# Optimization experiments

Hardware: AMD Instinct MI355X
Metric: run time of the kernel (lower is better)

The kernel has to match this reference:

```python
import jax, jax.numpy as jnp
import numpy as np

B, S, D, R, N_IN, N_PROC, K = 4, 4096, 1024, 128, 8, 32, 4

def setup_inputs() -> dict:
    key = jax.random.key(0)
    k1, k2, k3, k4, k5 = jax.random.split(key, 5)
    x = jax.random.normal(k1, (B, S, D), dtype=jnp.float32)
    input_weights = jax.random.uniform(k2, (B, S, N_IN), dtype=jnp.float32)
    process_indices = jax.random.randint(k3, (B, S, K), 0, N_PROC, dtype=jnp.int32)
    # params: orthogonal-ish init approximated by scaled gaussian
    input_neurons = jax.random.normal(k4, (N_IN, D, R), dtype=jnp.float32) / np.sqrt(D).astype(np.float32)
    process_neurons = jax.random.normal(k5, (N_PROC, R), dtype=jnp.float32)
    process_neurons = process_neurons / (jnp.linalg.norm(process_neurons, axis=-1, keepdims=True) + 1e-8)
    return {"x": x, "input_weights": input_weights, "process_indices": process_indices,
            "input_neurons": input_neurons, "process_neurons": process_neurons}

def reference(x, input_weights, process_indices, input_neurons, process_neurons):
    # soft routing over input neurons: project with all N_IN matrices, weight, sum
    all_proj = jnp.einsum('bsd,ndr->bsnr', x, input_neurons)      # [B,S,N_IN,R]
    y = jnp.einsum('bsnr,bsn->bsr', all_proj, input_weights)       # [B,S,R]
    # gather per-token Householder vectors: [B,S,K,R]
    selected_v = process_neurons[process_indices]
    # sequential chain of K Householder reflections via scan over the K axis
    def step(xc, v):
        # v: [B,S,R]
        v_norm_sq = jnp.sum(v * v, axis=-1, keepdims=True) + 1e-8
        vn = v / jnp.sqrt(v_norm_sq)
        vTx = jnp.sum(xc * vn, axis=-1, keepdims=True)
        return xc - 2.0 * vn * vTx, None
    out, _ = jax.lax.scan(step, y, jnp.moveaxis(selected_v, 2, 0))
    return out
```

## Files before the change

kernel.cpp:

```cpp
#include <hip/hip_runtime.h>
#include <hip/hip_bf16.h>
#include <stdint.h>

#define D_DIM 1024
#define R_DIM 128
#define NIN   8
#define M_TOT 16384

typedef unsigned short u16;
typedef __attribute__((ext_vector_type(4))) float f32x4;
typedef __attribute__((ext_vector_type(8))) __bf16 bf16x8;

__device__ __forceinline__ u16 f2b(float f) {
    union { float f; uint32_t u; } v; v.f = f;
    uint32_t r = (v.u + 0x7FFFu + ((v.u >> 16) & 1u)) >> 16;
    return (u16)r;
}

__device__ __forceinline__ void gload16(const void* g, void* l) {
    __builtin_amdgcn_global_load_lds(
        (const __attribute__((address_space(1))) uint32_t*)g,
        (__attribute__((address_space(3))) uint32_t*)l, 16, 0, 0);
}

#define SBAR  do { asm volatile("" ::: "memory"); __builtin_amdgcn_s_barrier(); asm volatile("" ::: "memory"); } while (0)
#define SBARL do { asm volatile("s_waitcnt lgkmcnt(0)" ::: "memory"); __builtin_amdgcn_s_barrier(); asm volatile("" ::: "memory"); } while (0)
#define WVMC(N) asm volatile("s_waitcnt vmcnt(" #N ")" ::: "memory")

__global__ __launch_bounds__(256)
void prep(const float* __restrict__ x, u16* __restrict__ xb,
          const float* __restrict__ inn, u16* __restrict__ Bt2) {
    if (blockIdx.x < 8192) {
        const size_t i = ((size_t)blockIdx.x * 256 + threadIdx.x) * 8;
        const f32x4 v0 = *(const f32x4*)&x[i];
        const f32x4 v1 = *(const f32x4*)&x[i + 4];
        union { u16 s[8]; uint4 v; } u;
#pragma unroll
        for (int q = 0; q < 4; ++q) { u.s[q] = f2b(v0[q]); u.s[4 + q] = f2b(v1[q]); }
        *(uint4*)&xb[i] = u.v;
    } else {
        const int idx = (int)blockIdx.x - 8192;
        const int n  = idx >> 4;
        const int d0 = (idx & 15) * 64;
        const int r   = threadIdx.x & 127;
        const int hf  = threadIdx.x >> 7;
        const size_t C = (size_t)((r >> 4) * 128 + n * 16 + (r & 15));
#pragma unroll
        for (int g = 0; g < 4; ++g) {
            const int gg = hf * 4 + g;
            union { u16 s[8]; uint4 v; } u;
#pragma unroll
            for (int jj = 0; jj < 8; ++jj)
                u.s[jj] = f2b(inn[((size_t)n * D_DIM + d0 + gg * 8 + jj) * R_DIM + r]);
            *(uint4*)&Bt2[C * D_DIM + d0 + gg * 8] = u.v;
        }
    }
}

__global__ __launch_bounds__(512, 2)
void gemm8(const u16* __restrict__ xb, const u16* __restrict__ Bt2,
           const float* __restrict__ iw, float* __restrict__ y) {
    __shared__ __align__(16) char smem[131072];
    char* As = smem;
    char* Bs = smem + 65536;

    const int tid  = threadIdx.x;
    const int wid  = tid >> 6, lane = tid & 63;
    const int wm = wid >> 2, wn = wid & 3;
    const int l15 = lane & 15, lq = lane >> 4;

    int wg = (int)blockIdx.x;
    wg = (wg & 7) * 32 + (wg >> 3);
    const int by = wg & 3, bx = wg >> 2;
    const int m0 = bx * 256, c0 = by * 256;

    const int sxor = ((tid & 7) * 16) ^ (((tid >> 3) & 7) << 4);
    const char* gA = (const char*)xb  + ((size_t)(m0 + (tid >> 3))) * 2048 + sxor;
    const char* gB = (const char*)Bt2 + ((size_t)(c0 + (tid >> 3))) * 2048 + sxor;

#define STA(T1, NB, Q) gload16(gA + (size_t)(Q) * 64 * 2048 + (size_t)(T1) * 128, As + (NB) * 32768 + (Q) * 8192 + tid * 16)
#define STB(T1, NB, C) gload16(gB + (size_t)(C) * 64 * 2048 + (size_t)(T1) * 128, Bs + (NB) * 32768 + (C) * 8192 + tid * 16)

#define RDA(DST, MH, CUR) \
    _Pragma("unroll") for (int i = 0; i < 4; ++i) \
    _Pragma("unroll") for (int kk = 0; kk < 2; ++kk) { \
        const int row = wm * 128 + (MH) * 64 + i * 16 + l15; \
        uint32_t off = (uint32_t)((CUR) * 32768 + row * 128 + kk * 64 + lq * 16); \
        off ^= (uint32_t)((row & 7) << 4); \
        DST[i][kk] = *(const bf16x8*)(As + off); }

#define RDB(NS, CUR) \
    _Pragma("unroll") for (int j = 0; j < 2; ++j) \
    _Pragma("unroll") for (int kk = 0; kk < 2; ++kk) { \
        const int cc = (NS) * 128 + wn * 32 + j * 16 + l15; \
        uint32_t off = (uint32_t)((CUR) * 32768 + cc * 128 + kk * 64 + lq * 16); \
        off ^= (uint32_t)((cc & 7) << 4); \
        b[NS][j][kk] = *(const bf16x8*)(Bs + off); }

#define MM(MH, NS, AF) do { \
    __builtin_amdgcn_s_setprio(1); \
    _Pragma("unroll") for (int i = 0; i < 4; ++i) \
    _Pragma("unroll") for (int j = 0; j < 2; ++j) \
    _Pragma("unroll") for (int kk = 0; kk < 2; ++kk) \
        acc[MH][NS][i][j] = __builtin_amdgcn_mfma_f32_16x16x32_bf16(AF[i][kk], b[NS][j][kk], acc[MH][NS][i][j], 0, 0, 0); \
    __builtin_amdgcn_s_setprio(0); } while (0)

#define TILE(T, CUR, NB) do { \
    const int t1_ = (T) + 1; const bool st_ = (t1_ < 16); \
    bf16x8 a0[4][2], a1[4][2], b[2][2][2]; \
     \
    RDA(a0, 0, CUR); RDB(0, CUR); \
    if (st_) { STA(t1_, NB, 0); STA(t1_, NB, 2); } \
    SBAR; MM(0, 0, a0); WVMC(4); SBAR; \
     \
    RDB(1, CUR); \
    if (st_) { STB(t1_, NB, 0); STB(t1_, NB, 1); } \
    SBAR; MM(0, 1, a0); WVMC(4); SBAR; \
     \
    RDA(a1, 1, CUR); \
    if (st_) { STB(t1_, NB, 2); STB(t1_, NB, 3); } \
    SBAR; MM(1, 0, a1); SBAR; \
     \
    if (st_) { STA(t1_, NB, 1); STA(t1_, NB, 3); } \
    SBAR; MM(1, 1, a1); WVMC(4); SBAR; \
} while (0)

    f32x4 acc[2][2][4][2] = {};

    STA(0, 0, 0); STA(0, 0, 2);
    STB(0, 0, 0); STB(0, 0, 1);
    STB(0, 0, 2); STB(0, 0, 3);
    STA(0, 0, 1); STA(0, 0, 3);
    WVMC(0); SBAR;

    for (int t = 0; t < 16; t += 2) {
        TILE(t, 0, 1);
        TILE(t + 1, 1, 0);
    }
    WVMC(0);

    float* P0 = (float*)smem;
    float* P1 = (float*)(smem + 34816);
    const float* wrow = iw + (size_t)m0 * NIN;

    float own[2][2][4][4];
#pragma unroll
    for (int mh = 0; mh < 2; ++mh)
#pragma unroll
        for (int i = 0; i < 4; ++i)
#pragma unroll
            for (int e = 0; e < 4; ++e) {
                const int row = wm * 128 + mh * 64 + i * 16 + lq * 4 + e;
                const float w0 = wrow[row * NIN + wn * 2 + 0];
                const float w1 = wrow[row * NIN + wn * 2 + 1];
#pragma unroll
                for (int ns = 0; ns < 2; ++ns)
                    own[mh][ns][i][e] = w0 * acc[mh][ns][i][0][e] + w1 * acc[mh][ns][i][1][e];
            }

#define PIX(NS, ROW) ((NS) * (256 * 17) + (ROW) * 17 + l15)
    SBAR;
    if (wn == 1 || wn == 3) {
        float* P = (wn == 1) ? P0 : P1;
#pragma unroll
        for (int mh = 0; mh < 2; ++mh)
#pragma unroll
            for (int ns = 0; ns < 2; ++ns)
#pragma unroll
                for (int i = 0; i < 4; ++i)
#pragma unroll
                    for (int e = 0; e < 4; ++e) {
                        const int row = wm * 128 + mh * 64 + i * 16 + lq * 4 + e;
                        P[PIX(ns, row)] = own[mh][ns][i][e];
                    }
    }
    SBARL;
    if (wn == 2) {
#pragma unroll
        for (int mh = 0; mh < 2; ++mh)
#pragma unroll
            for (int ns = 0; ns < 2; ++ns)
#pragma unroll
                for (int i = 0; i < 4; ++i)
#pragma unroll
                    for (int e = 0; e < 4; ++e) {
                        const int row = wm * 128 + mh * 64 + i * 16 + lq * 4 + e;
                        P1[PIX(ns, row)] += own[mh][ns][i][e];
                    }
    }
    SBARL;
    if (wn == 0) {
#pragma unroll
        for (int mh = 0; mh < 2; ++mh)
#pragma unroll
            for (int ns = 0; ns < 2; ++ns)
#pragma unroll
                for (int i = 0; i < 4; ++i)
#pragma unroll
                    for (int e = 0; e < 4; ++e) {
                        const int row = wm * 128 + mh * 64 + i * 16 + lq * 4 + e;
                        const float s = own[mh][ns][i][e] + P0[PIX(ns, row)] + P1[PIX(ns, row)];
                        y[(size_t)(m0 + row) * R_DIM + (2 * by + ns) * 16 + l15] = s;
                    }
    }
#undef PIX
#undef TILE
#undef MM
#undef RDB
#undef RDA
#undef STB
#undef STA
}

__global__ __launch_bounds__(512)
void house(float* __restrict__ y, const int* __restrict__ pidx,
           const float* __restrict__ pn) {
    const int tid = threadIdx.x;
    const int row = tid >> 3;
    const int cg  = tid & 7;
    const int c0  = cg * 16;
    const int tok = blockIdx.x * 64 + row;

    float yv[16];
#pragma unroll
    for (int q = 0; q < 4; ++q) {
        const f32x4 s = *(const f32x4*)&y[(size_t)tok * R_DIM + c0 + q * 4];
        yv[q * 4 + 0] = s[0]; yv[q * 4 + 1] = s[1]; yv[q * 4 + 2] = s[2]; yv[q * 4 + 3] = s[3];
    }

    const int4 idx4 = *(const int4*)&pidx[tok * 4];
    const int idxs[4] = { idx4.x, idx4.y, idx4.z, idx4.w };

#pragma unroll
    for (int k = 0; k < 4; ++k) {
        const float* vptr = &pn[(size_t)idxs[k] * R_DIM + c0];
        float v[16];
#pragma unroll
        for (int q = 0; q < 4; ++q) {
            const f32x4 vv4 = *(const f32x4*)&vptr[q * 4];
            v[q * 4 + 0] = vv4[0]; v[q * 4 + 1] = vv4[1];
            v[q * 4 + 2] = vv4[2]; v[q * 4 + 3] = vv4[3];
        }
        float vy = 0.f, vv = 0.f;
#pragma unroll
        for (int j = 0; j < 16; ++j) { vy += v[j] * yv[j]; vv += v[j] * v[j]; }
#pragma unroll
        for (int o = 1; o < 8; o <<= 1) {
            vy += __shfl_xor(vy, o);
            vv += __shfl_xor(vv, o);
        }
        const float s = 2.0f * vy / (vv + 1e-8f);
#pragma unroll
        for (int j = 0; j < 16; ++j) yv[j] -= s * v[j];
    }

#pragma unroll
    for (int q = 0; q < 4; ++q) {
        f32x4 o; o[0] = yv[q*4+0]; o[1] = yv[q*4+1]; o[2] = yv[q*4+2]; o[3] = yv[q*4+3];
        *(f32x4*)&y[(size_t)tok * R_DIM + c0 + q * 4] = o;
    }
}

extern "C" void kernel_launch(void* const* d_in, const int* in_sizes, int n_in,
                              void* d_out, int out_size, void* d_ws, size_t ws_size,
                              hipStream_t stream) {
    const float* x   = (const float*)d_in[0];
    const float* iw  = (const float*)d_in[1];
    const int*   pix = (const int*)d_in[2];
    const float* inn = (const float*)d_in[3];
    const float* pn  = (const float*)d_in[4];
    float* out = (float*)d_out;

    u16* xb  = (u16*)d_ws;
    u16* Bt2 = (u16*)((char*)d_ws + (size_t)(32 << 20));

    prep<<<8320, 256, 0, stream>>>(x, xb, inn, Bt2);
    gemm8<<<256, 512, 0, stream>>>(xb, Bt2, iw, out);
    house<<<256, 512, 0, stream>>>(out, pix, pn);
}
```

Baseline: 65.90 us.

## Fuse x conversion and Householder chain into GEMM with inter-block flags

Moves the fp32-to-bf16 conversion of x into the GEMM kernel: each of the four column blocks sharing a row tile converts one K quarter, publishes a flag, and starts its K loop at its own quarter. Before each later quarter it waits on the peer's flag, converting that quarter itself if the flag never appears. After writing y to a workspace buffer, blocks bump a per-row-tile counter, and the by==0 block spins until all four have finished, then runs the Householder reflections in place of the separate kernel. This removes two launches and one full pass over x, at the cost of spin-waits that assume co-residency, a memset of the flags, and Householder work concentrated in a quarter of the blocks.

```diff
diff --git a/kernel.cpp b/kernel.cpp
--- a/kernel.cpp
+++ b/kernel.cpp
@@ -27,40 +27,52 @@
 #define SBARL do { asm volatile("s_waitcnt lgkmcnt(0)" ::: "memory"); __builtin_amdgcn_s_barrier(); asm volatile("" ::: "memory"); } while (0)
 #define WVMC(N) asm volatile("s_waitcnt vmcnt(" #N ")" ::: "memory")
 
+__device__ __forceinline__ void conv_quarter(const float* __restrict__ x,
+                                             u16* __restrict__ xb,
+                                             int m0, int q, int tid) {
+    const size_t base = (size_t)m0 * D_DIM + (size_t)q * 256;
+#pragma unroll
+    for (int p = 0; p < 16; ++p) {
+        const int id  = p * 512 + tid;
+        const int row = id >> 5;
+        const int c8  = (id & 31) * 8;
+        const size_t off = base + (size_t)row * D_DIM + c8;
+        const f32x4 v0 = *(const f32x4*)&x[off];
+        const f32x4 v1 = *(const f32x4*)&x[off + 4];
+        union { u16 s[8]; uint4 v; } u;
+#pragma unroll
+        for (int qq = 0; qq < 4; ++qq) { u.s[qq] = f2b(v0[qq]); u.s[4 + qq] = f2b(v1[qq]); }
+        *(uint4*)&xb[off] = u.v;
+    }
+}
+
 __global__ __launch_bounds__(256)
-void prep(const float* __restrict__ x, u16* __restrict__ xb,
-          const float* __restrict__ inn, u16* __restrict__ Bt2) {
-    if (blockIdx.x < 8192) {
-        const size_t i = ((size_t)blockIdx.x * 256 + threadIdx.x) * 8;
-        const f32x4 v0 = *(const f32x4*)&x[i];
-        const f32x4 v1 = *(const f32x4*)&x[i + 4];
+void prep_b(const float* __restrict__ inn, u16* __restrict__ Bt2) {
+    const int idx = (int)blockIdx.x;
+    const int n  = idx >> 4;
+    const int d0 = (idx & 15) * 64;
+    const int r   = threadIdx.x & 127;
+    const int hf  = threadIdx.x >> 7;
+    const size_t C = (size_t)((r >> 4) * 128 + n * 16 + (r & 15));
+#pragma unroll
+    for (int g = 0; g < 4; ++g) {
+        const int gg = hf * 4 + g;
         union { u16 s[8]; uint4 v; } u;
 #pragma unroll
-        for (int q = 0; q < 4; ++q) { u.s[q] = f2b(v0[q]); u.s[4 + q] = f2b(v1[q]); }
-        *(uint4*)&xb[i] = u.v;
-    } else {
-        const int idx = (int)blockIdx.x - 8192;
-        const int n  = idx >> 4;
-        const int d0 = (idx & 15) * 64;
-        const int r   = threadIdx.x & 127;
-        const int hf  = threadIdx.x >> 7;
-        const size_t C = (size_t)((r >> 4) * 128 + n * 16 + (r & 15));
-#pragma unroll
-        for (int g = 0; g < 4; ++g) {
-            const int gg = hf * 4 + g;
-            union { u16 s[8]; uint4 v; } u;
-#pragma unroll
-            for (int jj = 0; jj < 8; ++jj)
-                u.s[jj] = f2b(inn[((size_t)n * D_DIM + d0 + gg * 8 + jj) * R_DIM + r]);
-            *(uint4*)&Bt2[C * D_DIM + d0 + gg * 8] = u.v;
-        }
+        for (int jj = 0; jj < 8; ++jj)
+            u.s[jj] = f2b(inn[((size_t)n * D_DIM + d0 + gg * 8 + jj) * R_DIM + r]);
+        *(uint4*)&Bt2[C * D_DIM + d0 + gg * 8] = u.v;
     }
 }
 
 __global__ __launch_bounds__(512, 2)
-void gemm8(const u16* __restrict__ xb, const u16* __restrict__ Bt2,
-           const float* __restrict__ iw, float* __restrict__ y) {
+void gemm_mega(const float* __restrict__ x, const u16* __restrict__ Bt2,
+               const float* __restrict__ iw, const int* __restrict__ pidx,
+               const float* __restrict__ pn, u16* __restrict__ xb,
+               float* __restrict__ y, int* __restrict__ qf, int* __restrict__ pcnt,
+               float* __restrict__ out) {
     __shared__ __align__(16) char smem[131072];
+    __shared__ int s_ok;
     char* As = smem;
     char* Bs = smem + 65536;
 
@@ -74,12 +86,39 @@
     const int by = wg & 3, bx = wg >> 2;
     const int m0 = bx * 256, c0 = by * 256;
 
+    conv_quarter(x, xb, m0, by, tid);
+    WVMC(0);
+    __threadfence();
+    __syncthreads();
+    if (tid == 0)
+        __hip_atomic_store(&qf[bx * 4 + by], 1, __ATOMIC_RELEASE, __HIP_MEMORY_SCOPE_AGENT);
+
+#define ENSQ(Q) do { \
+    if (tid == 0) { \
+        int ok_ = 0; \
+        for (int it_ = 0; it_ < 1000 && !ok_; ++it_) { \
+            ok_ = __hip_atomic_load(&qf[bx * 4 + (Q)], __ATOMIC_ACQUIRE, __HIP_MEMORY_SCOPE_AGENT); \
+            if (!ok_) __builtin_amdgcn_s_sleep(32); \
+        } \
+        s_ok = ok_; \
+    } \
+    __syncthreads(); \
+    if (!s_ok) {  \
+        conv_quarter(x, xb, m0, (Q), tid); \
+        WVMC(0); __threadfence(); __syncthreads(); \
+        if (tid == 0) __hip_atomic_store(&qf[bx * 4 + (Q)], 1, __ATOMIC_RELEASE, __HIP_MEMORY_SCOPE_AGENT); \
+        __syncthreads(); \
+    } \
+} while (0)
+
     const int sxor = ((tid & 7) * 16) ^ (((tid >> 3) & 7) << 4);
     const char* gA = (const char*)xb  + ((size_t)(m0 + (tid >> 3))) * 2048 + sxor;
     const char* gB = (const char*)Bt2 + ((size_t)(c0 + (tid >> 3))) * 2048 + sxor;
 
-#define STA(T1, NB, Q) gload16(gA + (size_t)(Q) * 64 * 2048 + (size_t)(T1) * 128, As + (NB) * 32768 + (Q) * 8192 + tid * 16)
-#define STB(T1, NB, C) gload16(gB + (size_t)(C) * 64 * 2048 + (size_t)(T1) * 128, Bs + (NB) * 32768 + (C) * 8192 + tid * 16)
+#define KOF(T) ((size_t)(((4 * by + (T)) & 15) * 128))
+
+#define STA(T1, NB, Q) gload16(gA + (size_t)(Q) * 64 * 2048 + KOF(T1), As + (NB) * 32768 + (Q) * 8192 + tid * 16)
+#define STB(T1, NB, C) gload16(gB + (size_t)(C) * 64 * 2048 + KOF(T1), Bs + (NB) * 32768 + (C) * 8192 + tid * 16)
 
 #define RDA(DST, MH, CUR) \
     _Pragma("unroll") for (int i = 0; i < 4; ++i) \
@@ -135,6 +174,8 @@
 
     for (int t = 0; t < 16; t += 2) {
         TILE(t, 0, 1);
+        if (((t + 2) & 3) == 0 && (t + 2) < 16)
+            ENSQ((by + ((t + 2) >> 2)) & 3);
         TILE(t + 1, 1, 0);
     }
     WVMC(0);
@@ -202,6 +243,64 @@
                         const float s = own[mh][ns][i][e] + P0[PIX(ns, row)] + P1[PIX(ns, row)];
                         y[(size_t)(m0 + row) * R_DIM + (2 * by + ns) * 16 + l15] = s;
                     }
+    }
+
+    WVMC(0);
+    __threadfence();
+    __syncthreads();
+    if (tid == 0)
+        __hip_atomic_fetch_add(&pcnt[bx], 1, __ATOMIC_ACQ_REL, __HIP_MEMORY_SCOPE_AGENT);
+
+    if (by != 0) return;
+
+    if (tid == 0) {
+        while (__hip_atomic_load(&pcnt[bx], __ATOMIC_ACQUIRE, __HIP_MEMORY_SCOPE_AGENT) < 4)
+            __builtin_amdgcn_s_sleep(8);
+        s_ok = 1;
+    }
+    __syncthreads();
+
+    const int hrow = tid >> 3;
+    const int cg   = tid & 7;
+    const int hc0  = cg * 16;
+#pragma unroll 1
+    for (int pass = 0; pass < 4; ++pass) {
+        const int tok = m0 + pass * 64 + hrow;
+        float yv[16];
+#pragma unroll
+        for (int q = 0; q < 4; ++q) {
+            const f32x4 s = *(const f32x4*)&y[(size_t)tok * R_DIM + hc0 + q * 4];
+            yv[q * 4 + 0] = s[0]; yv[q * 4 + 1] = s[1]; yv[q * 4 + 2] = s[2]; yv[q * 4 + 3] = s[3];
+        }
+        const int4 idx4 = *(const int4*)&pidx[tok * 4];
+        const int idxs[4] = { idx4.x, idx4.y, idx4.z, idx4.w };
+#pragma unroll
+        for (int k = 0; k < 4; ++k) {
+            const float* vptr = &pn[(size_t)idxs[k] * R_DIM + hc0];
+            float v[16];
+#pragma unroll
+            for (int q = 0; q < 4; ++q) {
+                const f32x4 vv4 = *(const f32x4*)&vptr[q * 4];
+                v[q * 4 + 0] = vv4[0]; v[q * 4 + 1] = vv4[1];
+                v[q * 4 + 2] = vv4[2]; v[q * 4 + 3] = vv4[3];
+            }
+            float vy = 0.f, vv = 0.f;
+#pragma unroll
+            for (int j = 0; j < 16; ++j) { vy += v[j] * yv[j]; vv += v[j] * v[j]; }
+#pragma unroll
+            for (int o = 1; o < 8; o <<= 1) {
+                vy += __shfl_xor(vy, o);
+                vv += __shfl_xor(vv, o);
+            }
+            const float s = 2.0f * vy / (vv + 1e-8f);
+#pragma unroll
+            for (int j = 0; j < 16; ++j) yv[j] -= s * v[j];
+        }
+#pragma unroll
+        for (int q = 0; q < 4; ++q) {
+            f32x4 o; o[0] = yv[q*4+0]; o[1] = yv[q*4+1]; o[2] = yv[q*4+2]; o[3] = yv[q*4+3];
+            *(f32x4*)&out[(size_t)tok * R_DIM + hc0 + q * 4] = o;
+        }
     }
 #undef PIX
 #undef TILE
@@ -210,55 +309,8 @@
 #undef RDA
 #undef STB
 #undef STA
-}
-
-__global__ __launch_bounds__(512)
-void house(float* __restrict__ y, const int* __restrict__ pidx,
-           const float* __restrict__ pn) {
-    const int tid = threadIdx.x;
-    const int row = tid >> 3;
-    const int cg  = tid & 7;
-    const int c0  = cg * 16;
-    const int tok = blockIdx.x * 64 + row;
-
-    float yv[16];
-#pragma unroll
-    for (int q = 0; q < 4; ++q) {
-        const f32x4 s = *(const f32x4*)&y[(size_t)tok * R_DIM + c0 + q * 4];
-        yv[q * 4 + 0] = s[0]; yv[q * 4 + 1] = s[1]; yv[q * 4 + 2] = s[2]; yv[q * 4 + 3] = s[3];
-    }
-
-    const int4 idx4 = *(const int4*)&pidx[tok * 4];
-    const int idxs[4] = { idx4.x, idx4.y, idx4.z, idx4.w };
-
-#pragma unroll
-    for (int k = 0; k < 4; ++k) {
-        const float* vptr = &pn[(size_t)idxs[k] * R_DIM + c0];
-        float v[16];
-#pragma unroll
-        for (int q = 0; q < 4; ++q) {
-            const f32x4 vv4 = *(const f32x4*)&vptr[q * 4];
-            v[q * 4 + 0] = vv4[0]; v[q * 4 + 1] = vv4[1];
-            v[q * 4 + 2] = vv4[2]; v[q * 4 + 3] = vv4[3];
-        }
-        float vy = 0.f, vv = 0.f;
-#pragma unroll
-        for (int j = 0; j < 16; ++j) { vy += v[j] * yv[j]; vv += v[j] * v[j]; }
-#pragma unroll
-        for (int o = 1; o < 8; o <<= 1) {
-            vy += __shfl_xor(vy, o);
-            vv += __shfl_xor(vv, o);
-        }
-        const float s = 2.0f * vy / (vv + 1e-8f);
-#pragma unroll
-        for (int j = 0; j < 16; ++j) yv[j] -= s * v[j];
-    }
-
-#pragma unroll
-    for (int q = 0; q < 4; ++q) {
-        f32x4 o; o[0] = yv[q*4+0]; o[1] = yv[q*4+1]; o[2] = yv[q*4+2]; o[3] = yv[q*4+3];
-        *(f32x4*)&y[(size_t)tok * R_DIM + c0 + q * 4] = o;
-    }
+#undef KOF
+#undef ENSQ
 }
 
 extern "C" void kernel_launch(void* const* d_in, const int* in_sizes, int n_in,
@@ -271,10 +323,13 @@
     const float* pn  = (const float*)d_in[4];
     float* out = (float*)d_out;
 
-    u16* xb  = (u16*)d_ws;
-    u16* Bt2 = (u16*)((char*)d_ws + (size_t)(32 << 20));
-
-    prep<<<8320, 256, 0, stream>>>(x, xb, inn, Bt2);
-    gemm8<<<256, 512, 0, stream>>>(xb, Bt2, iw, out);
-    house<<<256, 512, 0, stream>>>(out, pix, pn);
-}
+    u16*   xb   = (u16*)d_ws;
+    u16*   Bt2  = (u16*)((char*)d_ws + (size_t)(32 << 20));
+    float* y    = (float*)((char*)d_ws + (size_t)(34 << 20));
+    int*   qf   = (int*)((char*)d_ws + (size_t)(42 << 20));
+    int*   pcnt = qf + 256;
+
+    hipMemsetAsync(qf, 0, 2048, stream);
+    prep_b<<<128, 256, 0, stream>>>(inn, Bt2);
+    gemm_mega<<<256, 512, 0, stream>>>(x, Bt2, iw, pix, pn, xb, y, qf, pcnt, out);
+}
```

Measured after the change: 206.3 us. 213% more time.

## Fuse Householder chain into GEMM via per-row-tile atomic counter barrier

Applied to the files above, without the earlier changes.

Removes the separate house kernel launch. Each GEMM workgroup writes its column slice of y to a workspace buffer, increments a per-row-block counter, and spins until all four column workgroups of that 256-row block are done. It then applies the four Householder reflections to 64 of those rows and writes the final output. This saves a kernel launch and the gap between launches, in exchange for a memset, a spin-wait that needs all four sibling workgroups to be co-resident (256 blocks at 2 per CU makes that likely), and an extra y round-trip through the workspace.

```diff
diff --git a/kernel.cpp b/kernel.cpp
--- a/kernel.cpp
+++ b/kernel.cpp
@@ -59,7 +59,9 @@
 
 __global__ __launch_bounds__(512, 2)
 void gemm8(const u16* __restrict__ xb, const u16* __restrict__ Bt2,
-           const float* __restrict__ iw, float* __restrict__ y) {
+           const float* __restrict__ iw, const int* __restrict__ pidx,
+           const float* __restrict__ pn, float* __restrict__ y,
+           int* __restrict__ pcnt, float* __restrict__ out) {
     __shared__ __align__(16) char smem[131072];
     char* As = smem;
     char* Bs = smem + 65536;
@@ -203,6 +205,59 @@
                         y[(size_t)(m0 + row) * R_DIM + (2 * by + ns) * 16 + l15] = s;
                     }
     }
+
+    __threadfence();
+    __syncthreads();
+    if (tid == 0)
+        __hip_atomic_fetch_add(&pcnt[bx], 1, __ATOMIC_ACQ_REL, __HIP_MEMORY_SCOPE_AGENT);
+
+    if (tid == 0) {
+        while (__hip_atomic_load(&pcnt[bx], __ATOMIC_ACQUIRE, __HIP_MEMORY_SCOPE_AGENT) < 4)
+            __builtin_amdgcn_s_sleep(2);
+    }
+    __syncthreads();
+    (void)__hip_atomic_load(&pcnt[bx], __ATOMIC_ACQUIRE, __HIP_MEMORY_SCOPE_AGENT);
+
+    const int hrow = tid >> 3;
+    const int cg   = tid & 7;
+    const int hc0  = cg * 16;
+    const int tok  = m0 + by * 64 + hrow;
+
+    float yv[16];
+#pragma unroll
+    for (int q = 0; q < 4; ++q) {
+        const f32x4 s = *(const f32x4*)&y[(size_t)tok * R_DIM + hc0 + q * 4];
+        yv[q * 4 + 0] = s[0]; yv[q * 4 + 1] = s[1]; yv[q * 4 + 2] = s[2]; yv[q * 4 + 3] = s[3];
+    }
+    const int4 idx4 = *(const int4*)&pidx[tok * 4];
+    const int idxs[4] = { idx4.x, idx4.y, idx4.z, idx4.w };
+#pragma unroll
+    for (int k = 0; k < 4; ++k) {
+        const float* vptr = &pn[(size_t)idxs[k] * R_DIM + hc0];
+        float v[16];
+#pragma unroll
+        for (int q = 0; q < 4; ++q) {
+            const f32x4 vv4 = *(const f32x4*)&vptr[q * 4];
+            v[q * 4 + 0] = vv4[0]; v[q * 4 + 1] = vv4[1];
+            v[q * 4 + 2] = vv4[2]; v[q * 4 + 3] = vv4[3];
+        }
+        float vy = 0.f, vv = 0.f;
+#pragma unroll
+        for (int j = 0; j < 16; ++j) { vy += v[j] * yv[j]; vv += v[j] * v[j]; }
+#pragma unroll
+        for (int o = 1; o < 8; o <<= 1) {
+            vy += __shfl_xor(vy, o);
+            vv += __shfl_xor(vv, o);
+        }
+        const float s = 2.0f * vy / (vv + 1e-8f);
+#pragma unroll
+        for (int j = 0; j < 16; ++j) yv[j] -= s * v[j];
+    }
+#pragma unroll
+    for (int q = 0; q < 4; ++q) {
+        f32x4 o; o[0] = yv[q*4+0]; o[1] = yv[q*4+1]; o[2] = yv[q*4+2]; o[3] = yv[q*4+3];
+        *(f32x4*)&out[(size_t)tok * R_DIM + hc0 + q * 4] = o;
+    }
 #undef PIX
 #undef TILE
 #undef MM
@@ -210,55 +265,6 @@
 #undef RDA
 #undef STB
 #undef STA
-}
-
-__global__ __launch_bounds__(512)
-void house(float* __restrict__ y, const int* __restrict__ pidx,
-           const float* __restrict__ pn) {
-    const int tid = threadIdx.x;
-    const int row = tid >> 3;
-    const int cg  = tid & 7;
-    const int c0  = cg * 16;
-    const int tok = blockIdx.x * 64 + row;
-
-    float yv[16];
-#pragma unroll
-    for (int q = 0; q < 4; ++q) {
-        const f32x4 s = *(const f32x4*)&y[(size_t)tok * R_DIM + c0 + q * 4];
-        yv[q * 4 + 0] = s[0]; yv[q * 4 + 1] = s[1]; yv[q * 4 + 2] = s[2]; yv[q * 4 + 3] = s[3];
-    }
-
-    const int4 idx4 = *(const int4*)&pidx[tok * 4];
-    const int idxs[4] = { idx4.x, idx4.y, idx4.z, idx4.w };
-
-#pragma unroll
-    for (int k = 0; k < 4; ++k) {
-        const float* vptr = &pn[(size_t)idxs[k] * R_DIM + c0];
-        float v[16];
-#pragma unroll
-        for (int q = 0; q < 4; ++q) {
-            const f32x4 vv4 = *(const f32x4*)&vptr[q * 4];
-            v[q * 4 + 0] = vv4[0]; v[q * 4 + 1] = vv4[1];
-            v[q * 4 + 2] = vv4[2]; v[q * 4 + 3] = vv4[3];
-        }
-        float vy = 0.f, vv = 0.f;
-#pragma unroll
-        for (int j = 0; j < 16; ++j) { vy += v[j] * yv[j]; vv += v[j] * v[j]; }
-#pragma unroll
-        for (int o = 1; o < 8; o <<= 1) {
-            vy += __shfl_xor(vy, o);
-            vv += __shfl_xor(vv, o);
-        }
-        const float s = 2.0f * vy / (vv + 1e-8f);
-#pragma unroll
-        for (int j = 0; j < 16; ++j) yv[j] -= s * v[j];
-    }
-
-#pragma unroll
-    for (int q = 0; q < 4; ++q) {
-        f32x4 o; o[0] = yv[q*4+0]; o[1] = yv[q*4+1]; o[2] = yv[q*4+2]; o[3] = yv[q*4+3];
-        *(f32x4*)&y[(size_t)tok * R_DIM + c0 + q * 4] = o;
-    }
 }
 
 extern "C" void kernel_launch(void* const* d_in, const int* in_sizes, int n_in,
@@ -271,10 +277,12 @@
     const float* pn  = (const float*)d_in[4];
     float* out = (float*)d_out;
 
-    u16* xb  = (u16*)d_ws;
-    u16* Bt2 = (u16*)((char*)d_ws + (size_t)(32 << 20));
-
+    u16*   xb   = (u16*)d_ws;
+    u16*   Bt2  = (u16*)((char*)d_ws + (size_t)(32 << 20));
+    float* y    = (float*)((char*)d_ws + (size_t)(34 << 20));
+    int*   pcnt = (int*)((char*)d_ws + (size_t)(42 << 20));
+
+    hipMemsetAsync(pcnt, 0, 1024, stream);
     prep<<<8320, 256, 0, stream>>>(x, xb, inn, Bt2);
-    gemm8<<<256, 512, 0, stream>>>(xb, Bt2, iw, out);
-    house<<<256, 512, 0, stream>>>(out, pix, pn);
-}
+    gemm8<<<256, 512, 0, stream>>>(xb, Bt2, iw, pix, pn, y, pcnt, out);
+}
```

Result: slower. 135.0 us (+104.8%).
